# Kernel tuning notes

Measured on AMD Instinct MI355X. Metric: run time of the kernel, lower is better.

## Reference

```python
import jax, jax.numpy as jnp
import numpy as np

HEADS = 4
DIM_HEAD = 128

def setup_inputs() -> dict:
    key = jax.random.key(0)
    k1, k2, k3, k4 = jax.random.split(key, 4)
    scale = DIM_HEAD ** -0.5
    return {
        "fmap": jax.random.normal(k1, (16, 512, 32, 32), dtype=jnp.float32),
        "w_qkv": jax.random.normal(k2, (1536, 512), dtype=jnp.float32) * 0.02,
        "height": jax.random.normal(k3, (32, DIM_HEAD), dtype=jnp.float32) * scale,
        "width": jax.random.normal(k4, (32, DIM_HEAD), dtype=jnp.float32) * scale,
    }

def reference(fmap, w_qkv, height, width):
    b, c, h, w = fmap.shape
    scale = DIM_HEAD ** -0.5
    # 1x1 conv == channel GEMM: (b, 3*heads*dim_head, h, w)
    qkv = jnp.einsum('bchw,oc->bohw', fmap, w_qkv)
    # split into q,k,v and reshape to (b, heads, seq, dim_head)
    qkv = qkv.reshape(b, 3, HEADS, DIM_HEAD, h * w)
    q, k, v = (jnp.transpose(qkv[:, i], (0, 1, 3, 2)) for i in range(3))
    # content logits
    sim = jnp.einsum('bhid,bhjd->bhij', q, k) * scale
    # absolute positional bias: emb[(x,y)] = height[x] + width[y]
    emb = (height[:, None, :] + width[None, :, :]).reshape(h * w, DIM_HEAD)
    sim = sim + jnp.einsum('bhid,jd->bhij', q, emb) * scale
    attn = jax.nn.softmax(sim, axis=-1)
    out = jnp.einsum('bhij,bhjd->bhid', attn, v)  # (b, heads, seq, d)
    out = jnp.transpose(out, (0, 1, 3, 2)).reshape(b, HEADS * DIM_HEAD, h, w)
    return out
```

## Files before the change

kernel.cpp:

```cpp
#include <hip/hip_runtime.h>
#include <math.h>

#define HEADS 4
#define DIMH  128
#define NB    16
#define CIN   512
#define SEQ   1024
#define OTOT  1536
#define KQ    (CIN / 8)

typedef __attribute__((ext_vector_type(8)))  short bf16x8;
typedef __attribute__((ext_vector_type(4)))  short bf16x4;
typedef __attribute__((ext_vector_type(4)))  float f32x4;
typedef __attribute__((ext_vector_type(16))) float f32x16;

#define MFMA16(a,b,c) __builtin_amdgcn_mfma_f32_16x16x32_bf16(a,b,c,0,0,0)
#define MFMA32(a,b,c) __builtin_amdgcn_mfma_f32_32x32x16_bf16(a,b,c,0,0,0)

__device__ __forceinline__ short f2bf(float f) {
    unsigned u = __builtin_bit_cast(unsigned, f);
    u = (u + 0x7FFFu + ((u >> 16) & 1u)) >> 16;
    return (short)u;
}
__device__ __forceinline__ unsigned pk2(float lo, float hi) {
    return __builtin_amdgcn_perm(__builtin_bit_cast(unsigned, hi),
                                 __builtin_bit_cast(unsigned, lo), 0x07060302u);
}
union PF8 { unsigned u[4]; bf16x8 v; };

__device__ __forceinline__ void gll16(const short* g, short* l) {
    __builtin_amdgcn_global_load_lds(
        (const __attribute__((address_space(1))) unsigned*)g,
        (__attribute__((address_space(3))) unsigned*)l,
        16, 0, 0);
}

__global__ __launch_bounds__(256) void convert_all(const float* __restrict__ F,
                                                   const float* __restrict__ W,
                                                   short* __restrict__ FT2,
                                                   short* __restrict__ Wb2) {
    const int kq = blockIdx.y;
    if (blockIdx.z == NB) {
        const int o = blockIdx.x * 256 + threadIdx.x;
        float4 v0 = *(const float4*)&W[(size_t)o * CIN + kq * 8];
        float4 v1 = *(const float4*)&W[(size_t)o * CIN + kq * 8 + 4];
        bf16x8 pk = { f2bf(v0.x), f2bf(v0.y), f2bf(v0.z), f2bf(v0.w),
                      f2bf(v1.x), f2bf(v1.y), f2bf(v1.z), f2bf(v1.w) };
        *(bf16x8*)&Wb2[((size_t)kq * OTOT + o) * 8] = pk;
        return;
    }
    if (blockIdx.x >= 4) return;
    const int s = blockIdx.x * 256 + threadIdx.x;
    const int b = blockIdx.z;
    const float* src = F + ((size_t)b * CIN + kq * 8) * SEQ + s;
    float v[8];
    #pragma unroll
    for (int i = 0; i < 8; ++i) v[i] = src[(size_t)i * SEQ];
    bf16x8 pk = { f2bf(v[0]), f2bf(v[1]), f2bf(v[2]), f2bf(v[3]),
                  f2bf(v[4]), f2bf(v[5]), f2bf(v[6]), f2bf(v[7]) };
    *(bf16x8*)&FT2[(((size_t)b * KQ + kq) * SEQ + s) * 8] = pk;
}

__global__ __launch_bounds__(256, 3) void qkv_gemm(
    const short* __restrict__ Wb2, const short* __restrict__ FT2,
    const float* __restrict__ height, const float* __restrict__ width,
    short* __restrict__ Qo, short* __restrict__ Kfo, short* __restrict__ Vfo)
{
    __shared__ short As[2][4 * 128 * 8];
    __shared__ short Bs[2][4 * 128 * 8];

    const int L  = blockIdx.x;
    const int x8 = L & 7, m = L >> 3;
    const int g  = x8 + 8 * (m / 12);
    const int oy = m % 12;
    const int b  = g >> 3, sx = g & 7;
    const int o0 = oy * 128, s0 = sx * 128;

    const int t = threadIdx.x, l = t & 63, w = t >> 6;
    const int quad = l >> 4, ln = l & 15;
    const int wrow = (w >> 1) * 64, wcol = (w & 1) * 64;

#define STAGE(ks, buf) { \
    _Pragma("unroll") for (int r = 0; r < 4; ++r) { \
        const int task = r * 4 + w; \
        const int p = task >> 1, hf = task & 1; \
        if (p < 4) { \
            const short* gsrc = Wb2 + (((size_t)((ks) * 4 + p) * OTOT) + o0 + hf * 64 + l) * 8; \
            gll16(gsrc, &As[buf][(p * 128 + hf * 64) * 8]); \
        } else { \
            const short* gsrc = FT2 + ((((size_t)b * KQ + (ks) * 4 + (p - 4)) * SEQ) + s0 + hf * 64 + l) * 8; \
            gll16(gsrc, &Bs[buf][((p - 4) * 128 + hf * 64) * 8]); \
        } \
    } }

    f32x4 acc[4][4] = {};

    STAGE(0, 0);
    __syncthreads();

    for (int ks = 0; ks < 16; ++ks) {
        const int cb = ks & 1;
        if (ks < 15) STAGE(ks + 1, cb ^ 1);
        const short* Ab = &As[cb][0];
        const short* Bb = &Bs[cb][0];
        bf16x8 af[4], bfr[4];
        #pragma unroll
        for (int i = 0; i < 4; ++i)
            af[i]  = *(const bf16x8*)&Ab[((size_t)quad * 128 + wrow + i * 16 + ln) * 8];
        #pragma unroll
        for (int j = 0; j < 4; ++j)
            bfr[j] = *(const bf16x8*)&Bb[((size_t)quad * 128 + wcol + j * 16 + ln) * 8];
        #pragma unroll
        for (int i = 0; i < 4; ++i)
            #pragma unroll
            for (int j = 0; j < 4; ++j)
                acc[i][j] = MFMA16(af[i], bfr[j], acc[i][j]);
        __syncthreads();
    }

    const int sec = o0 >> 9;
    const int h   = (o0 >> 7) & 3;
    const size_t bh = (size_t)b * HEADS + h;

    if (sec == 0) {
        const float qs = 0.08838834764831845f * 1.4426950408889634f;
        #pragma unroll
        for (int ti = 0; ti < 4; ++ti) {
            int d = wrow + ti * 16 + quad * 4;
            #pragma unroll
            for (int tj = 0; tj < 4; ++tj) {
                int s = s0 + wcol + tj * 16 + ln;
                f32x4 a = acc[ti][tj];
                bf16x4 pk4 = { f2bf(a[0]*qs), f2bf(a[1]*qs), f2bf(a[2]*qs), f2bf(a[3]*qs) };
                *(bf16x4*)&Qo[(bh * SEQ + s) * DIMH + d] = pk4;
            }
        }
    } else if (sec == 1) {
        #pragma unroll
        for (int ti = 0; ti < 4; ++ti) {
            int d = wrow + ti * 16 + quad * 4;
            #pragma unroll
            for (int tj = 0; tj < 4; ++tj) {
                int s = s0 + wcol + tj * 16 + ln;
                float4 hv = *(const float4*)&height[(size_t)(s >> 5) * DIMH + d];
                float4 wv = *(const float4*)&width[(size_t)(s & 31) * DIMH + d];
                f32x4 a = acc[ti][tj];
                bf16x4 pk4 = { f2bf(a[0] + hv.x + wv.x), f2bf(a[1] + hv.y + wv.y),
                               f2bf(a[2] + hv.z + wv.z), f2bf(a[3] + hv.w + wv.w) };
                *(bf16x4*)&Kfo[(((size_t)bh * 16 + (d >> 3)) * SEQ + s) * 8 + (d & 7)] = pk4;
            }
        }
    } else {
        const int slot = ((ln >> 2) & 1) * 8 + (ln & 3) + ((ln >> 3) << 2);
        #pragma unroll
        for (int ti = 0; ti < 4; ++ti) {
            int d = wrow + ti * 16 + quad * 4;
            #pragma unroll
            for (int tj = 0; tj < 4; ++tj) {
                int s = s0 + wcol + tj * 16 + ln;
                size_t vb = (((size_t)bh * 64 + (s >> 4)) * DIMH) * 16 + slot;
                f32x4 a = acc[ti][tj];
                #pragma unroll
                for (int r = 0; r < 4; ++r)
                    Vfo[vb + (size_t)(d + r) * 16] = f2bf(a[r]);
            }
        }
    }
}

#define BQ 128
#define BJ 64
#define KSTR 136

#define ATTN_ITER(ti, DO_QK, DO_PRE, DO_BAR)                                        \
{                                                                                   \
    const int rd = (((ti) + 1) & 3) * (BJ * KSTR);                                  \
    const int wr = (((ti) + 3) & 3) * (BJ * KSTR);                                  \
    const short* vp0 = Vlane + (size_t)((ti) * 4) * (DIMH * 16);                    \
    bf16x8 vr[4][4];                                                                \
    _Pragma("unroll") for (int gi = 0; gi < 2; ++gi)                                \
      _Pragma("unroll") for (int dc = 0; dc < 4; ++dc)                              \
        vr[gi][dc] = *(const bf16x8*)(vp0 + (size_t)gi * (DIMH * 16) + dc * 32 * 16);\
    int4 kreg[4];                                                                   \
    if (DO_PRE) {                                                                   \
        _Pragma("unroll") for (int p = 0; p < 4; ++p)                               \
            kreg[p] = *(const int4*)(Kg + ((size_t)(p * 4 + w) * SEQ + ((ti) + 3) * BJ + l) * 8); \
    }                                                                               \
    PF8 pf[4];                                                                      \
    _Pragma("unroll") for (int g = 0; g < 4; ++g) {                                 \
        const f32x16& Sh = (g & 2) ? S1 : S0;                                       \
        const int kk = g & 1;                                                       \
        _Pragma("unroll") for (int mm = 0; mm < 4; ++mm) {                          \
            float ea = __builtin_amdgcn_exp2f(Sh[kk * 8 + 2 * mm]);                 \
            float eb = __builtin_amdgcn_exp2f(Sh[kk * 8 + 2 * mm + 1]);             \
            psum += ea + eb;                                                        \
            pf[g].u[mm] = pk2(ea, eb);                                              \
        }                                                                           \
    }                                                                               \
    _Pragma("unroll") for (int gi = 2; gi < 4; ++gi)                                \
      _Pragma("unroll") for (int dc = 0; dc < 4; ++dc)                              \
        vr[gi][dc] = *(const bf16x8*)(vp0 + (size_t)gi * (DIMH * 16) + dc * 32 * 16);\
    if (DO_QK) {                                                                    \
        S0 = (f32x16){}; S1 = (f32x16){};                                           \
        _Pragma("unroll") for (int kc = 0; kc < 8; ++kc) {                          \
            bf16x8 k0 = *(const bf16x8*)&Ks[rd + c31 * KSTR + kc * 16 + h * 8];     \
            bf16x8 k1 = *(const bf16x8*)&Ks[rd + (32 + c31) * KSTR + kc * 16 + h * 8]; \
            S0 = MFMA32(k0, qf[kc], S0);                                            \
            S1 = MFMA32(k1, qf[kc], S1);                                            \
        }                                                                           \
    }                                                                               \
    _Pragma("unroll") for (int g = 0; g < 4; ++g)                                   \
        _Pragma("unroll") for (int dc = 0; dc < 4; ++dc)                            \
            O[dc] = MFMA32(vr[g][dc], pf[g].v, O[dc]);                              \
    if (DO_PRE) {                                                                   \
        _Pragma("unroll") for (int p = 0; p < 4; ++p)                               \
            *(int4*)&Ks[wr + l * KSTR + (p * 4 + w) * 8] = kreg[p];                 \
    }                                                                               \
    if (DO_BAR) __syncthreads();                                                    \
}

__global__ __launch_bounds__(256, 2) void attn(
    const short* __restrict__ Q, const short* __restrict__ Kf,
    const short* __restrict__ Vf, float* __restrict__ out)
{
    __shared__ short Ks[4 * BJ * KSTR];

    const int t = threadIdx.x, l = t & 63, w = t >> 6;
    const int h = l >> 5, c31 = l & 31;

    const int L = blockIdx.x;
    const int x = L & 7, inner = L >> 3;
    const int bh = x * 8 + (inner >> 3);
    const int q0 = (inner & 7) * BQ;
    const size_t obase = (size_t)bh * DIMH * SEQ;

    bf16x8 qf[8];
    {
        const short* Qp = Q + ((size_t)bh * SEQ + (q0 + w * 32 + c31)) * DIMH + h * 8;
        #pragma unroll
        for (int kc = 0; kc < 8; ++kc)
            qf[kc] = *(const bf16x8*)(Qp + kc * 16);
    }

    const short* Kg = Kf + (size_t)bh * 16 * SEQ * 8;
    const short* Vlane = Vf + (size_t)bh * 64 * (DIMH * 16) + (c31 * 16 + h * 8);

    f32x16 O[4] = {};
    float psum = 0.f;

    {
        int4 k0[4], k1[4], k2[4];
        #pragma unroll
        for (int p = 0; p < 4; ++p) {
            k0[p] = *(const int4*)(Kg + ((size_t)(p * 4 + w) * SEQ + l) * 8);
            k1[p] = *(const int4*)(Kg + ((size_t)(p * 4 + w) * SEQ + BJ + l) * 8);
            k2[p] = *(const int4*)(Kg + ((size_t)(p * 4 + w) * SEQ + 2 * BJ + l) * 8);
        }
        #pragma unroll
        for (int p = 0; p < 4; ++p) {
            *(int4*)&Ks[l * KSTR + (p * 4 + w) * 8] = k0[p];
            *(int4*)&Ks[1 * (BJ * KSTR) + l * KSTR + (p * 4 + w) * 8] = k1[p];
            *(int4*)&Ks[2 * (BJ * KSTR) + l * KSTR + (p * 4 + w) * 8] = k2[p];
        }
    }
    __syncthreads();

    f32x16 S0 = {}, S1 = {};
    #pragma unroll
    for (int kc = 0; kc < 8; ++kc) {
        bf16x8 k0 = *(const bf16x8*)&Ks[c31 * KSTR + kc * 16 + h * 8];
        bf16x8 k1 = *(const bf16x8*)&Ks[(32 + c31) * KSTR + kc * 16 + h * 8];
        S0 = MFMA32(k0, qf[kc], S0);
        S1 = MFMA32(k1, qf[kc], S1);
    }
    __syncthreads();

    for (int p = 0; p < 6; ++p) {
        const int t0 = 2 * p;
        ATTN_ITER(t0,     true, true, false);
        ATTN_ITER(t0 + 1, true, true, true);
    }
    ATTN_ITER(12, true, true,  false);
    ATTN_ITER(13, true, false, true);
    ATTN_ITER(14, true, false, false);
    ATTN_ITER(15, false, false, false);

    psum += __shfl_xor(psum, 32);
    float linv = 1.0f / psum;

    #pragma unroll
    for (int dc = 0; dc < 4; ++dc)
        #pragma unroll
        for (int r = 0; r < 16; ++r) {
            int d = dc * 32 + (r & 3) + 8 * (r >> 2) + 4 * h;
            out[obase + (size_t)d * SEQ + q0 + w * 32 + c31] = O[dc][r] * linv;
        }
}

extern "C" void kernel_launch(void* const* d_in, const int* in_sizes, int n_in,
                              void* d_out, int out_size, void* d_ws, size_t ws_size,
                              hipStream_t stream) {
    const float* fmap   = (const float*)d_in[0];
    const float* w_qkv  = (const float*)d_in[1];
    const float* height = (const float*)d_in[2];
    const float* width  = (const float*)d_in[3];
    float* outp = (float*)d_out;

    const size_t n_ft  = (size_t)NB * SEQ * CIN;
    const size_t n_w   = (size_t)OTOT * CIN;
    const size_t n_qkv = (size_t)NB * HEADS * SEQ * DIMH;

    short* FT2 = (short*)d_ws;
    short* Wb2 = FT2 + n_ft;
    short* Qb  = Wb2 + n_w;
    short* Kfb = Qb + n_qkv;
    short* Vfb = Kfb + n_qkv;

    convert_all<<<dim3(6, KQ, NB + 1), 256, 0, stream>>>(fmap, w_qkv, FT2, Wb2);
    qkv_gemm<<<dim3(8 * 12 * NB), 256, 0, stream>>>(
        Wb2, FT2, height, width, Qb, Kfb, Vfb);
    attn<<<dim3(NB * HEADS * (SEQ / BQ)), 256, 0, stream>>>(Qb, Kfb, Vfb, outp);
}
```

Measured before the change: 166.3 us.

## Fuse fmap bf16 conversion into QKV GEMM staging via register prefetch

Removes the separate fmap conversion pass and its bf16 workspace buffer. The GEMM now loads fp32 fmap directly into registers for the next k-step, converts after the MFMA block, and writes the result to LDS. Weights still use async global-to-LDS loads. This saves a full write and reread of the converted feature map. In exchange, each fmap tile is read in fp32 by all twelve output-row blocks, and register pressure rises.

```diff
diff --git a/kernel.cpp b/kernel.cpp
--- a/kernel.cpp
+++ b/kernel.cpp
@@ -35,34 +35,19 @@
         16, 0, 0);
 }
 
-__global__ __launch_bounds__(256) void convert_all(const float* __restrict__ F,
-                                                   const float* __restrict__ W,
-                                                   short* __restrict__ FT2,
-                                                   short* __restrict__ Wb2) {
+__global__ __launch_bounds__(256) void convert_w(const float* __restrict__ W,
+                                                 short* __restrict__ Wb2) {
     const int kq = blockIdx.y;
-    if (blockIdx.z == NB) {
-        const int o = blockIdx.x * 256 + threadIdx.x;
-        float4 v0 = *(const float4*)&W[(size_t)o * CIN + kq * 8];
-        float4 v1 = *(const float4*)&W[(size_t)o * CIN + kq * 8 + 4];
-        bf16x8 pk = { f2bf(v0.x), f2bf(v0.y), f2bf(v0.z), f2bf(v0.w),
-                      f2bf(v1.x), f2bf(v1.y), f2bf(v1.z), f2bf(v1.w) };
-        *(bf16x8*)&Wb2[((size_t)kq * OTOT + o) * 8] = pk;
-        return;
-    }
-    if (blockIdx.x >= 4) return;
-    const int s = blockIdx.x * 256 + threadIdx.x;
-    const int b = blockIdx.z;
-    const float* src = F + ((size_t)b * CIN + kq * 8) * SEQ + s;
-    float v[8];
-    #pragma unroll
-    for (int i = 0; i < 8; ++i) v[i] = src[(size_t)i * SEQ];
-    bf16x8 pk = { f2bf(v[0]), f2bf(v[1]), f2bf(v[2]), f2bf(v[3]),
-                  f2bf(v[4]), f2bf(v[5]), f2bf(v[6]), f2bf(v[7]) };
-    *(bf16x8*)&FT2[(((size_t)b * KQ + kq) * SEQ + s) * 8] = pk;
+    const int o = blockIdx.x * 256 + threadIdx.x;
+    float4 v0 = *(const float4*)&W[(size_t)o * CIN + kq * 8];
+    float4 v1 = *(const float4*)&W[(size_t)o * CIN + kq * 8 + 4];
+    bf16x8 pk = { f2bf(v0.x), f2bf(v0.y), f2bf(v0.z), f2bf(v0.w),
+                  f2bf(v1.x), f2bf(v1.y), f2bf(v1.z), f2bf(v1.w) };
+    *(bf16x8*)&Wb2[((size_t)kq * OTOT + o) * 8] = pk;
 }
 
 __global__ __launch_bounds__(256, 3) void qkv_gemm(
-    const short* __restrict__ Wb2, const short* __restrict__ FT2,
+    const short* __restrict__ Wb2, const float* __restrict__ F,
     const float* __restrict__ height, const float* __restrict__ width,
     short* __restrict__ Qo, short* __restrict__ Kfo, short* __restrict__ Vfo)
 {
@@ -80,27 +65,36 @@
     const int quad = l >> 4, ln = l & 15;
     const int wrow = (w >> 1) * 64, wcol = (w & 1) * 64;
 
-#define STAGE(ks, buf) { \
-    _Pragma("unroll") for (int r = 0; r < 4; ++r) { \
-        const int task = r * 4 + w; \
-        const int p = task >> 1, hf = task & 1; \
-        if (p < 4) { \
-            const short* gsrc = Wb2 + (((size_t)((ks) * 4 + p) * OTOT) + o0 + hf * 64 + l) * 8; \
-            gll16(gsrc, &As[buf][(p * 128 + hf * 64) * 8]); \
-        } else { \
-            const short* gsrc = FT2 + ((((size_t)b * KQ + (ks) * 4 + (p - 4)) * SEQ) + s0 + hf * 64 + l) * 8; \
-            gll16(gsrc, &Bs[buf][((p - 4) * 128 + hf * 64) * 8]); \
-        } \
-    } }
+    const int pa = w >> 1, hfw = w & 1;
+    float fv0[8], fv1[8];
+
+#define STAGE_ISSUE(ks, buf) { \
+    gll16(Wb2 + (((size_t)((ks) * 4 + pa) * OTOT) + o0 + hfw * 64 + l) * 8, \
+          &As[buf][(pa * 128 + hfw * 64) * 8]); \
+    gll16(Wb2 + (((size_t)((ks) * 4 + 2 + pa) * OTOT) + o0 + hfw * 64 + l) * 8, \
+          &As[buf][((2 + pa) * 128 + hfw * 64) * 8]); \
+    const float* f0 = F + ((size_t)b * CIN + ((ks) * 4 + pa) * 8) * SEQ + (s0 + hfw * 64 + l); \
+    const float* f1 = F + ((size_t)b * CIN + ((ks) * 4 + 2 + pa) * 8) * SEQ + (s0 + hfw * 64 + l); \
+    _Pragma("unroll") for (int i = 0; i < 8; ++i) fv0[i] = f0[(size_t)i * SEQ]; \
+    _Pragma("unroll") for (int i = 0; i < 8; ++i) fv1[i] = f1[(size_t)i * SEQ]; }
+
+#define STAGE_WRITE(buf) { \
+    bf16x8 pk0 = { f2bf(fv0[0]), f2bf(fv0[1]), f2bf(fv0[2]), f2bf(fv0[3]), \
+                   f2bf(fv0[4]), f2bf(fv0[5]), f2bf(fv0[6]), f2bf(fv0[7]) }; \
+    bf16x8 pk1 = { f2bf(fv1[0]), f2bf(fv1[1]), f2bf(fv1[2]), f2bf(fv1[3]), \
+                   f2bf(fv1[4]), f2bf(fv1[5]), f2bf(fv1[6]), f2bf(fv1[7]) }; \
+    *(bf16x8*)&Bs[buf][(pa * 128 + hfw * 64 + l) * 8] = pk0; \
+    *(bf16x8*)&Bs[buf][((2 + pa) * 128 + hfw * 64 + l) * 8] = pk1; }
 
     f32x4 acc[4][4] = {};
 
-    STAGE(0, 0);
+    STAGE_ISSUE(0, 0);
+    STAGE_WRITE(0);
     __syncthreads();
 
     for (int ks = 0; ks < 16; ++ks) {
         const int cb = ks & 1;
-        if (ks < 15) STAGE(ks + 1, cb ^ 1);
+        if (ks < 15) STAGE_ISSUE(ks + 1, cb ^ 1);
         const short* Ab = &As[cb][0];
         const short* Bb = &Bs[cb][0];
         bf16x8 af[4], bfr[4];
@@ -115,6 +109,7 @@
             #pragma unroll
             for (int j = 0; j < 4; ++j)
                 acc[i][j] = MFMA16(af[i], bfr[j], acc[i][j]);
+        if (ks < 15) STAGE_WRITE(cb ^ 1);
         __syncthreads();
     }
 
@@ -306,18 +301,16 @@
     const float* width  = (const float*)d_in[3];
     float* outp = (float*)d_out;
 
-    const size_t n_ft  = (size_t)NB * SEQ * CIN;
     const size_t n_w   = (size_t)OTOT * CIN;
     const size_t n_qkv = (size_t)NB * HEADS * SEQ * DIMH;
 
-    short* FT2 = (short*)d_ws;
-    short* Wb2 = FT2 + n_ft;
+    short* Wb2 = (short*)d_ws;
     short* Qb  = Wb2 + n_w;
     short* Kfb = Qb + n_qkv;
     short* Vfb = Kfb + n_qkv;
 
-    convert_all<<<dim3(6, KQ, NB + 1), 256, 0, stream>>>(fmap, w_qkv, FT2, Wb2);
+    convert_w<<<dim3(6, KQ), 256, 0, stream>>>(w_qkv, Wb2);
     qkv_gemm<<<dim3(8 * 12 * NB), 256, 0, stream>>>(
-        Wb2, FT2, height, width, Qb, Kfb, Vfb);
+        Wb2, fmap, height, width, Qb, Kfb, Vfb);
     attn<<<dim3(NB * HEADS * (SEQ / BQ)), 256, 0, stream>>>(Qb, Kfb, Vfb, outp);
 }
```

New measurement: 175.1 us. 5.3% more time.

## Compute two output-channel tiles per QKV GEMM block to reuse B loads

Applied to the files above, without the earlier changes.

Each qkv_gemm block now computes two 128-row output-channel tiles (yy and yy+6) against the same 128-column activation tile, halving the grid to 768 blocks. This reuses each staged B tile from shared memory across twice the MFMA work and cuts global/LDS traffic for the feature map. In exchange, accumulator registers double (128 floats per thread) and shared memory grows, which may reduce occupancy under the launch_bounds(256,3) setting and leaves fewer blocks to fill the GPU.

```diff
diff --git a/kernel.cpp b/kernel.cpp
--- a/kernel.cpp
+++ b/kernel.cpp
@@ -66,34 +66,35 @@
     const float* __restrict__ height, const float* __restrict__ width,
     short* __restrict__ Qo, short* __restrict__ Kfo, short* __restrict__ Vfo)
 {
-    __shared__ short As[2][4 * 128 * 8];
+    __shared__ short As[2][2 * 4 * 128 * 8];
     __shared__ short Bs[2][4 * 128 * 8];
 
     const int L  = blockIdx.x;
     const int x8 = L & 7, m = L >> 3;
-    const int g  = x8 + 8 * (m / 12);
-    const int oy = m % 12;
+    const int g  = x8 + 8 * (m / 6);
+    const int yy = m % 6;
     const int b  = g >> 3, sx = g & 7;
-    const int o0 = oy * 128, s0 = sx * 128;
+    const int s0 = sx * 128;
 
     const int t = threadIdx.x, l = t & 63, w = t >> 6;
     const int quad = l >> 4, ln = l & 15;
     const int wrow = (w >> 1) * 64, wcol = (w & 1) * 64;
 
 #define STAGE(ks, buf) { \
-    _Pragma("unroll") for (int r = 0; r < 4; ++r) { \
+    _Pragma("unroll") for (int r = 0; r < 6; ++r) { \
         const int task = r * 4 + w; \
-        const int p = task >> 1, hf = task & 1; \
-        if (p < 4) { \
-            const short* gsrc = Wb2 + (((size_t)((ks) * 4 + p) * OTOT) + o0 + hf * 64 + l) * 8; \
-            gll16(gsrc, &As[buf][(p * 128 + hf * 64) * 8]); \
+        if (task < 16) { \
+            const int sl = task >> 3, p = (task >> 1) & 3, hf = task & 1; \
+            const short* gsrc = Wb2 + (((size_t)((ks) * 4 + p) * OTOT) + (yy + 6 * sl) * 128 + hf * 64 + l) * 8; \
+            gll16(gsrc, &As[buf][((sl * 4 + p) * 128 + hf * 64) * 8]); \
         } else { \
-            const short* gsrc = FT2 + ((((size_t)b * KQ + (ks) * 4 + (p - 4)) * SEQ) + s0 + hf * 64 + l) * 8; \
-            gll16(gsrc, &Bs[buf][((p - 4) * 128 + hf * 64) * 8]); \
+            const int p = (task - 16) >> 1, hf = task & 1; \
+            const short* gsrc = FT2 + ((((size_t)b * KQ + (ks) * 4 + p) * SEQ) + s0 + hf * 64 + l) * 8; \
+            gll16(gsrc, &Bs[buf][(p * 128 + hf * 64) * 8]); \
         } \
     } }
 
-    f32x4 acc[4][4] = {};
+    f32x4 acc[2][4][4] = {};
 
     STAGE(0, 0);
     __syncthreads();
@@ -103,66 +104,74 @@
         if (ks < 15) STAGE(ks + 1, cb ^ 1);
         const short* Ab = &As[cb][0];
         const short* Bb = &Bs[cb][0];
-        bf16x8 af[4], bfr[4];
-        #pragma unroll
-        for (int i = 0; i < 4; ++i)
-            af[i]  = *(const bf16x8*)&Ab[((size_t)quad * 128 + wrow + i * 16 + ln) * 8];
+        bf16x8 af[2][4], bfr[4];
+        #pragma unroll
+        for (int sl = 0; sl < 2; ++sl)
+            #pragma unroll
+            for (int i = 0; i < 4; ++i)
+                af[sl][i] = *(const bf16x8*)&Ab[(((sl * 4 + quad) * 128) + wrow + i * 16 + ln) * 8];
         #pragma unroll
         for (int j = 0; j < 4; ++j)
             bfr[j] = *(const bf16x8*)&Bb[((size_t)quad * 128 + wcol + j * 16 + ln) * 8];
         #pragma unroll
-        for (int i = 0; i < 4; ++i)
-            #pragma unroll
-            for (int j = 0; j < 4; ++j)
-                acc[i][j] = MFMA16(af[i], bfr[j], acc[i][j]);
+        for (int sl = 0; sl < 2; ++sl)
+            #pragma unroll
+            for (int i = 0; i < 4; ++i)
+                #pragma unroll
+                for (int j = 0; j < 4; ++j)
+                    acc[sl][i][j] = MFMA16(af[sl][i], bfr[j], acc[sl][i][j]);
         __syncthreads();
     }
 
-    const int sec = o0 >> 9;
-    const int h   = (o0 >> 7) & 3;
-    const size_t bh = (size_t)b * HEADS + h;
-
-    if (sec == 0) {
-        const float qs = 0.08838834764831845f * 1.4426950408889634f;
-        #pragma unroll
-        for (int ti = 0; ti < 4; ++ti) {
-            int d = wrow + ti * 16 + quad * 4;
-            #pragma unroll
-            for (int tj = 0; tj < 4; ++tj) {
-                int s = s0 + wcol + tj * 16 + ln;
-                f32x4 a = acc[ti][tj];
-                bf16x4 pk4 = { f2bf(a[0]*qs), f2bf(a[1]*qs), f2bf(a[2]*qs), f2bf(a[3]*qs) };
-                *(bf16x4*)&Qo[(bh * SEQ + s) * DIMH + d] = pk4;
+    #pragma unroll
+    for (int sl = 0; sl < 2; ++sl) {
+        const int o0  = (yy + 6 * sl) * 128;
+        const int sec = o0 >> 9;
+        const int h   = (o0 >> 7) & 3;
+        const size_t bh = (size_t)b * HEADS + h;
+
+        if (sec == 0) {
+            const float qs = 0.08838834764831845f * 1.4426950408889634f;
+            #pragma unroll
+            for (int ti = 0; ti < 4; ++ti) {
+                int d = wrow + ti * 16 + quad * 4;
+                #pragma unroll
+                for (int tj = 0; tj < 4; ++tj) {
+                    int s = s0 + wcol + tj * 16 + ln;
+                    f32x4 a = acc[sl][ti][tj];
+                    bf16x4 pk4 = { f2bf(a[0]*qs), f2bf(a[1]*qs), f2bf(a[2]*qs), f2bf(a[3]*qs) };
+                    *(bf16x4*)&Qo[(bh * SEQ + s) * DIMH + d] = pk4;
+                }
             }
-        }
-    } else if (sec == 1) {
-        #pragma unroll
-        for (int ti = 0; ti < 4; ++ti) {
-            int d = wrow + ti * 16 + quad * 4;
-            #pragma unroll
-            for (int tj = 0; tj < 4; ++tj) {
-                int s = s0 + wcol + tj * 16 + ln;
-                float4 hv = *(const float4*)&height[(size_t)(s >> 5) * DIMH + d];
-                float4 wv = *(const float4*)&width[(size_t)(s & 31) * DIMH + d];
-                f32x4 a = acc[ti][tj];
-                bf16x4 pk4 = { f2bf(a[0] + hv.x + wv.x), f2bf(a[1] + hv.y + wv.y),
-                               f2bf(a[2] + hv.z + wv.z), f2bf(a[3] + hv.w + wv.w) };
-                *(bf16x4*)&Kfo[(((size_t)bh * 16 + (d >> 3)) * SEQ + s) * 8 + (d & 7)] = pk4;
+        } else if (sec == 1) {
+            #pragma unroll
+            for (int ti = 0; ti < 4; ++ti) {
+                int d = wrow + ti * 16 + quad * 4;
+                #pragma unroll
+                for (int tj = 0; tj < 4; ++tj) {
+                    int s = s0 + wcol + tj * 16 + ln;
+                    float4 hv = *(const float4*)&height[(size_t)(s >> 5) * DIMH + d];
+                    float4 wv = *(const float4*)&width[(size_t)(s & 31) * DIMH + d];
+                    f32x4 a = acc[sl][ti][tj];
+                    bf16x4 pk4 = { f2bf(a[0] + hv.x + wv.x), f2bf(a[1] + hv.y + wv.y),
+                                   f2bf(a[2] + hv.z + wv.z), f2bf(a[3] + hv.w + wv.w) };
+                    *(bf16x4*)&Kfo[(((size_t)bh * 16 + (d >> 3)) * SEQ + s) * 8 + (d & 7)] = pk4;
+                }
             }
-        }
-    } else {
-        const int slot = ((ln >> 2) & 1) * 8 + (ln & 3) + ((ln >> 3) << 2);
-        #pragma unroll
-        for (int ti = 0; ti < 4; ++ti) {
-            int d = wrow + ti * 16 + quad * 4;
-            #pragma unroll
-            for (int tj = 0; tj < 4; ++tj) {
-                int s = s0 + wcol + tj * 16 + ln;
-                size_t vb = (((size_t)bh * 64 + (s >> 4)) * DIMH) * 16 + slot;
-                f32x4 a = acc[ti][tj];
+        } else {
+            const int slot = ((ln >> 2) & 1) * 8 + (ln & 3) + ((ln >> 3) << 2);
+            #pragma unroll
+            for (int ti = 0; ti < 4; ++ti) {
+                int d = wrow + ti * 16 + quad * 4;
                 #pragma unroll
-                for (int r = 0; r < 4; ++r)
-                    Vfo[vb + (size_t)(d + r) * 16] = f2bf(a[r]);
+                for (int tj = 0; tj < 4; ++tj) {
+                    int s = s0 + wcol + tj * 16 + ln;
+                    size_t vb = (((size_t)bh * 64 + (s >> 4)) * DIMH) * 16 + slot;
+                    f32x4 a = acc[sl][ti][tj];
+                    #pragma unroll
+                    for (int r = 0; r < 4; ++r)
+                        Vfo[vb + (size_t)(d + r) * 16] = f2bf(a[r]);
+                }
             }
         }
     }
@@ -317,7 +326,7 @@
     short* Vfb = Kfb + n_qkv;
 
     convert_all<<<dim3(6, KQ, NB + 1), 256, 0, stream>>>(fmap, w_qkv, FT2, Wb2);
-    qkv_gemm<<<dim3(8 * 12 * NB), 256, 0, stream>>>(
+    qkv_gemm<<<dim3(8 * 6 * NB), 256, 0, stream>>>(
         Wb2, FT2, height, width, Qb, Kfb, Vfb);
     attn<<<dim3(NB * HEADS * (SEQ / BQ)), 256, 0, stream>>>(Qb, Kfb, Vfb, outp);
 }
```

New measurement: 171.9 us. 1.03x slower.
